# Optimization experiments

Measured on AMD Instinct MI355X. Metric: run time of the kernel, lower is better.

The kernel has to match this reference:

```python
import jax, jax.numpy as jnp
import numpy as np


def _step(state):
    # state: [B, H, W] in {0.0, 1.0}
    p = jnp.pad(state, ((0, 0), (1, 1), (1, 1)))
    neighbors = (p[:, :-2, :-2] + p[:, :-2, 1:-1] + p[:, :-2, 2:]
                 + p[:, 1:-1, :-2] + p[:, 1:-1, 2:]
                 + p[:, 2:, :-2] + p[:, 2:, 1:-1] + p[:, 2:, 2:])
    alive = state > 0.5
    survives = alive & ((neighbors == 2.0) | (neighbors == 3.0))
    born = (~alive) & (neighbors == 3.0)
    return jnp.where(survives | born, jnp.ones_like(state), jnp.zeros_like(state))


def setup_inputs() -> dict:
    key = jax.random.key(0)
    k1, k2 = jax.random.split(key)
    B, H, W = 32, 1024, 1024
    # Binary occupancy grids in {0.0, 1.0} as the rule expects
    initial_state = (jax.random.uniform(k1, (B, H, W)) > 0.5).astype(jnp.float32)
    target = (jax.random.uniform(k2, (B, H, W)) > 0.5).astype(jnp.float32)
    return {"initial_state": initial_state, "target": target, "generations": 8}


def reference(initial_state, target, generations):
    state = initial_state
    for _ in range(generations):  # small fixed unroll, strict sequential dependency
        state = _step(state)
    error = state - target
    loss = jnp.mean(error * error)
    live_cells = state.sum()
    max_abs_error = jnp.abs(error).max()
    return loss, state, target, live_cells, max_abs_error
```

## Files before the change

kernel.cpp:

```cpp
#include <hip/hip_runtime.h>
#include <cstdint>

typedef unsigned long long u64;

#define BATCH   32
#define H       1024
#define W       1024
#define WPR     16
#define TR      64
#define HALO    8
#define BR      (TR + 2*HALO)
#define BRP     (BR + 2)
#define WP      (WPR + 2)
#define THREADS 512
#define NWAVES  (THREADS/64)
#define GENS    8
#define GRID    (BATCH * (H / TR))
#define NTOT    33554432ULL

__device__ __forceinline__ u64 shflxor64(u64 v, int m) {
    return (u64)__shfl_xor((long long)v, m, 64);
}

__device__ __forceinline__ void hrow(u64 L, u64 C, u64 R, u64& o, u64& t) {
    u64 wv = (C << 1) | (L >> 63);
    u64 ev = (C >> 1) | (R << 63);
    o = wv ^ C ^ ev;
    t = (wv & C) | (ev & (wv ^ C));
}

__device__ __forceinline__ u64 life_next(u64 oA, u64 tA, u64 oB, u64 tB,
                                         u64 oC, u64 tC, u64 mid) {
    u64 oa = oA ^ oB ^ oC;
    u64 oc = (oA & oB) | (oC & (oA ^ oB));
    u64 ts = tA ^ tB ^ tC;
    u64 tc = (tA & tB) | (tC & (tA ^ tB));
    u64 b1 = oc ^ ts;
    u64 cc = oc & ts;
    u64 b2 = cc ^ tc;
    u64 b3 = cc & tc;
    u64 eq3 = oa & b1 & ~(b2 | b3);
    u64 eq4 = (~oa) & (~b1) & b2 & (~b3);
    return eq3 | (mid & eq4);
}

__global__ __launch_bounds__(THREADS)
void gol_fused(const float* __restrict__ in_state,
               const float* __restrict__ target,
               float* __restrict__ out,
               u64* __restrict__ counters)
{
    __shared__ u64 buf[2][BRP][WP];
    __shared__ u64 tbits[TR][WPR + 1];
    __shared__ unsigned int wsum[NWAVES];

    const int tile = blockIdx.x;
    const int tpb  = H / TR;
    const int b    = tile / tpb;
    const int r0   = (tile - b * tpb) * TR;

    const int tid  = threadIdx.x;
    const int wave = tid >> 6;
    const int lane = tid & 63;

    for (int i = tid; i < 2 * BRP * WP; i += THREADS)
        ((u64*)buf)[i] = 0ULL;
    if (tid < TR) tbits[tid][WPR] = 0ULL;
    __syncthreads();

    const size_t boff = (size_t)b * H * W;
    const float* inb  = in_state + boff;

    const int sub   = lane & 15;
    const int wsub  = lane >> 4;

    for (int br = wave; br < BR; br += NWAVES) {
        int gr = r0 - HALO + br;
        if (gr < 0 || gr >= H) continue;
        const float4* rowp4 = (const float4*)(inb + (size_t)gr * W);
        #pragma unroll
        for (int g = 0; g < 4; ++g) {
            float4 f = rowp4[g * 64 + lane];
            u64 nib = (u64)((f.x > 0.5f) | ((f.y > 0.5f) << 1) |
                            ((f.z > 0.5f) << 2) | ((f.w > 0.5f) << 3));
            u64 v = nib << (sub * 4);
            v |= shflxor64(v, 1);
            v |= shflxor64(v, 2);
            v |= shflxor64(v, 4);
            v |= shflxor64(v, 8);
            if (sub == 0)
                buf[0][br + 1][g * 4 + wsub + 1] = v;
        }
    }

    for (int lr = wave; lr < TR; lr += NWAVES) {
        const float4* rowp4 = (const float4*)(target + boff + (size_t)(r0 + lr) * W);
        #pragma unroll
        for (int g = 0; g < 4; ++g) {
            float4 f = rowp4[g * 64 + lane];
            u64 nib = (u64)((f.x > 0.5f) | ((f.y > 0.5f) << 1) |
                            ((f.z > 0.5f) << 2) | ((f.w > 0.5f) << 3));
            u64 v = nib << (sub * 4);
            v |= shflxor64(v, 1);
            v |= shflxor64(v, 2);
            v |= shflxor64(v, 4);
            v |= shflxor64(v, 8);
            if (sub == 0)
                tbits[lr][g * 4 + wsub] = v;
        }
    }
    __syncthreads();

    int cur = 0;
    for (int step = 0; step < GENS; ++step) {
        const int lo     = step + 1;
        const int npairs = 39 - step;
        const int items  = npairs * WPR;
        for (int idx = tid; idx < items; idx += THREADS) {
            int pr  = idx >> 4;
            int c   = (idx & 15) + 1;
            int br0 = lo + 2 * pr;
            int r   = br0 + 1;

            u64 o0, t0, o1, t1, o2, t2, o3, t3, mB, mC;
            { u64 L = buf[cur][r-1][c-1], C = buf[cur][r-1][c], R = buf[cur][r-1][c+1];
              hrow(L, C, R, o0, t0); }
            { u64 L = buf[cur][r  ][c-1], C = buf[cur][r  ][c], R = buf[cur][r  ][c+1];
              hrow(L, C, R, o1, t1); mB = C; }
            { u64 L = buf[cur][r+1][c-1], C = buf[cur][r+1][c], R = buf[cur][r+1][c+1];
              hrow(L, C, R, o2, t2); mC = C; }
            { u64 L = buf[cur][r+2][c-1], C = buf[cur][r+2][c], R = buf[cur][r+2][c+1];
              hrow(L, C, R, o3, t3); }

            u64 n0 = life_next(o0, t0, o1, t1, o2, t2, mB);
            u64 n1 = life_next(o1, t1, o2, t2, o3, t3, mC);

            int gr0 = r0 - HALO + br0;
            buf[cur ^ 1][r    ][c] = (gr0     >= 0 && gr0     < H) ? n0 : 0ULL;
            buf[cur ^ 1][r + 1][c] = (gr0 + 1 >= 0 && gr0 + 1 < H) ? n1 : 0ULL;
        }
        __syncthreads();
        cur ^= 1;
    }

    float* o_state = out + 1;
    float* o_tgt   = out + 1 + NTOT;

    unsigned int mism = 0, live = 0;
    for (int lr = wave; lr < TR; lr += NWAVES) {
        int br = HALO + lr;
        int gr = r0 + lr;
        size_t rowbase = boff + (size_t)gr * W;
        const u64* wrow = &buf[cur][br + 1][1];
        const u64* trow = &tbits[lr][0];
        float* osrow = o_state + rowbase;
        float* otrow = o_tgt + rowbase;
        #pragma unroll
        for (int g = 0; g < 4; ++g) {
            int k = g * 64 + lane;
            if (k < 255) {
                int bitbase = 4 * k + 3;
                int w0 = bitbase >> 6;
                int sh = bitbase & 63;
                u64 slo = wrow[w0], shi = wrow[w0 + 1];
                u64 tlo = trow[w0], thi = trow[w0 + 1];
                unsigned sb = (unsigned)(((slo >> sh) | (shi << (64 - sh))) & 0xFULL);
                unsigned tb = (unsigned)(((tlo >> sh) | (thi << (64 - sh))) & 0xFULL);
                mism += (unsigned)__popc(sb ^ tb);
                live += (unsigned)__popc(sb);
                float4 sv, tv;
                sv.x = (float)(sb & 1u);
                sv.y = (float)((sb >> 1) & 1u);
                sv.z = (float)((sb >> 2) & 1u);
                sv.w = (float)((sb >> 3) & 1u);
                tv.x = (float)(tb & 1u);
                tv.y = (float)((tb >> 1) & 1u);
                tv.z = (float)((tb >> 2) & 1u);
                tv.w = (float)((tb >> 3) & 1u);
                *(float4*)(osrow + bitbase) = sv;
                *(float4*)(otrow + bitbase) = tv;
            } else {
                u64 sfirst = wrow[0],  slast = wrow[15];
                u64 tfirst = trow[0],  tlast = trow[15];
                unsigned shb = (unsigned)(sfirst & 7ULL);
                unsigned thb = (unsigned)(tfirst & 7ULL);
                unsigned stb = (unsigned)(slast >> 63);
                unsigned ttb = (unsigned)(tlast >> 63);
                mism += (unsigned)__popc(shb ^ thb) + (stb ^ ttb);
                live += (unsigned)__popc(shb) + stb;
                osrow[0]    = (float)(shb & 1u);
                osrow[1]    = (float)((shb >> 1) & 1u);
                osrow[2]    = (float)((shb >> 2) & 1u);
                osrow[1023] = (float)stb;
                otrow[0]    = (float)(thb & 1u);
                otrow[1]    = (float)((thb >> 1) & 1u);
                otrow[2]    = (float)((thb >> 2) & 1u);
                otrow[1023] = (float)ttb;
            }
        }
    }

    unsigned int comb = (mism << 16) | live;
    #pragma unroll
    for (int m = 1; m < 64; m <<= 1)
        comb += (unsigned int)__shfl_xor((int)comb, m, 64);
    if (lane == 0) wsum[wave] = comb;
    __syncthreads();

    if (tid == 0) {
        unsigned int bm = 0, bl = 0;
        #pragma unroll
        for (int i = 0; i < NWAVES; ++i) {
            bm += wsum[i] >> 16;
            bl += wsum[i] & 0xFFFFu;
        }
        atomicAdd(counters, ((u64)bm << 32) | (u64)bl);
    }
}

__global__ void gol_finalize(const u64* __restrict__ counters,
                             float* __restrict__ out)
{
    u64 c = *counters;
    unsigned int mism = (unsigned int)(c >> 32);
    unsigned int live = (unsigned int)(c & 0xFFFFFFFFULL);
    out[0]            = (float)((double)mism / (double)NTOT);
    out[1 + 2*NTOT]   = (float)live;
    out[2 + 2*NTOT]   = (mism > 0) ? 1.0f : 0.0f;
}

extern "C" void kernel_launch(void* const* d_in, const int* in_sizes, int n_in,
                              void* d_out, int out_size, void* d_ws, size_t ws_size,
                              hipStream_t stream) {
    (void)in_sizes; (void)n_in; (void)out_size; (void)ws_size;
    const float* in_state = (const float*)d_in[0];
    const float* target   = (const float*)d_in[1];
    float* out = (float*)d_out;
    u64* counters = (u64*)d_ws;

    hipMemsetAsync(d_ws, 0, sizeof(u64), stream);

    gol_fused<<<dim3(GRID), dim3(THREADS), 0, stream>>>(in_state, target, out, counters);
    gol_finalize<<<1, 1, 0, stream>>>(counters, out);
}
```

Baseline: 461.0 us.

## Pack bits via ballot, overlap target loads with generations, nontemporal stores

```diff
diff --git a/kernel.cpp b/kernel.cpp
--- a/kernel.cpp
+++ b/kernel.cpp
@@ -2,6 +2,7 @@
 #include <cstdint>
 
 typedef unsigned long long u64;
+typedef float f32x4 __attribute__((ext_vector_type(4)));
 
 #define BATCH   32
 #define H       1024
@@ -18,10 +19,6 @@
 #define GRID    (BATCH * (H / TR))
 #define NTOT    33554432ULL
 
-__device__ __forceinline__ u64 shflxor64(u64 v, int m) {
-    return (u64)__shfl_xor((long long)v, m, 64);
-}
-
 __device__ __forceinline__ void hrow(u64 L, u64 C, u64 R, u64& o, u64& t) {
     u64 wv = (C << 1) | (L >> 63);
     u64 ev = (C >> 1) | (R << 63);
@@ -70,49 +67,33 @@
 
     const size_t boff = (size_t)b * H * W;
     const float* inb  = in_state + boff;
-
-    const int sub   = lane & 15;
-    const int wsub  = lane >> 4;
+    const float* tgb  = target + boff;
 
     for (int br = wave; br < BR; br += NWAVES) {
         int gr = r0 - HALO + br;
         if (gr < 0 || gr >= H) continue;
-        const float4* rowp4 = (const float4*)(inb + (size_t)gr * W);
-        #pragma unroll
-        for (int g = 0; g < 4; ++g) {
-            float4 f = rowp4[g * 64 + lane];
-            u64 nib = (u64)((f.x > 0.5f) | ((f.y > 0.5f) << 1) |
-                            ((f.z > 0.5f) << 2) | ((f.w > 0.5f) << 3));
-            u64 v = nib << (sub * 4);
-            v |= shflxor64(v, 1);
-            v |= shflxor64(v, 2);
-            v |= shflxor64(v, 4);
-            v |= shflxor64(v, 8);
-            if (sub == 0)
-                buf[0][br + 1][g * 4 + wsub + 1] = v;
-        }
-    }
-
-    for (int lr = wave; lr < TR; lr += NWAVES) {
-        const float4* rowp4 = (const float4*)(target + boff + (size_t)(r0 + lr) * W);
-        #pragma unroll
-        for (int g = 0; g < 4; ++g) {
-            float4 f = rowp4[g * 64 + lane];
-            u64 nib = (u64)((f.x > 0.5f) | ((f.y > 0.5f) << 1) |
-                            ((f.z > 0.5f) << 2) | ((f.w > 0.5f) << 3));
-            u64 v = nib << (sub * 4);
-            v |= shflxor64(v, 1);
-            v |= shflxor64(v, 2);
-            v |= shflxor64(v, 4);
-            v |= shflxor64(v, 8);
-            if (sub == 0)
-                tbits[lr][g * 4 + wsub] = v;
-        }
+        const float* rowp = inb + (size_t)gr * W;
+        u64 myw = 0;
+        #pragma unroll
+        for (int g = 0; g < 16; ++g) {
+            float f = rowp[g * 64 + lane];
+            u64 m = __ballot(f > 0.5f);
+            if (lane == g) myw = m;
+        }
+        if (lane < 16)
+            buf[0][br + 1][lane + 1] = myw;
     }
     __syncthreads();
 
     int cur = 0;
     for (int step = 0; step < GENS; ++step) {
+        const int lr = step * NWAVES + wave;
+        const float* trowp = tgb + (size_t)(r0 + lr) * W;
+        float tf[16];
+        #pragma unroll
+        for (int g = 0; g < 16; ++g)
+            tf[g] = trowp[g * 64 + lane];
+
         const int lo     = step + 1;
         const int npairs = 39 - step;
         const int items  = npairs * WPR;
@@ -139,6 +120,18 @@
             buf[cur ^ 1][r    ][c] = (gr0     >= 0 && gr0     < H) ? n0 : 0ULL;
             buf[cur ^ 1][r + 1][c] = (gr0 + 1 >= 0 && gr0 + 1 < H) ? n1 : 0ULL;
         }
+
+        {
+            u64 myw = 0;
+            #pragma unroll
+            for (int g = 0; g < 16; ++g) {
+                u64 m = __ballot(tf[g] > 0.5f);
+                if (lane == g) myw = m;
+            }
+            if (lane < 16)
+                tbits[lr][lane] = myw;
+        }
+
         __syncthreads();
         cur ^= 1;
     }
@@ -168,7 +161,7 @@
                 unsigned tb = (unsigned)(((tlo >> sh) | (thi << (64 - sh))) & 0xFULL);
                 mism += (unsigned)__popc(sb ^ tb);
                 live += (unsigned)__popc(sb);
-                float4 sv, tv;
+                f32x4 sv, tv;
                 sv.x = (float)(sb & 1u);
                 sv.y = (float)((sb >> 1) & 1u);
                 sv.z = (float)((sb >> 2) & 1u);
@@ -177,8 +170,8 @@
                 tv.y = (float)((tb >> 1) & 1u);
                 tv.z = (float)((tb >> 2) & 1u);
                 tv.w = (float)((tb >> 3) & 1u);
-                *(float4*)(osrow + bitbase) = sv;
-                *(float4*)(otrow + bitbase) = tv;
+                __builtin_nontemporal_store(sv, (f32x4*)(osrow + bitbase));
+                __builtin_nontemporal_store(tv, (f32x4*)(otrow + bitbase));
             } else {
                 u64 sfirst = wrow[0],  slast = wrow[15];
                 u64 tfirst = trow[0],  tlast = trow[15];
```

New measurement: 467.5 us. Within noise of the previous version (+1.4%).
